# Kernel optimization log

Hardware: AMD Instinct MI355X
Metric: run time of the kernel (lower is better)

## Reference

```python
import jax, jax.numpy as jnp
import numpy as np

SINK = 4          # sink_size: tokens never evicted
MAX_CACHE = 8192  # sink_size + window_size
H = 32            # n_heads
HD = 128          # head_dim
D = H * HD        # d_model


def setup_inputs() -> dict:
    key = jax.random.key(0)
    ks = jax.random.split(key, 7)
    x = jax.random.normal(ks[0], (1, 1, D), dtype=jnp.float32)
    cached_k = jax.random.normal(ks[1], (1, H, MAX_CACHE, HD), dtype=jnp.float32)
    cached_v = jax.random.normal(ks[2], (1, H, MAX_CACHE, HD), dtype=jnp.float32)
    scale = 0.02
    Wq = jax.random.normal(ks[3], (D, D), dtype=jnp.float32) * scale
    Wk = jax.random.normal(ks[4], (D, D), dtype=jnp.float32) * scale
    Wv = jax.random.normal(ks[5], (D, D), dtype=jnp.float32) * scale
    Wo = jax.random.normal(ks[6], (D, D), dtype=jnp.float32) * scale
    return {"x": x, "cached_k": cached_k, "cached_v": cached_v,
            "Wq": Wq, "Wk": Wk, "Wv": Wv, "Wo": Wo}


def reference(x, cached_k, cached_v, Wq, Wk, Wv, Wo):
    """One StreamingLLM decode step with a full sink+window KV cache.

    x:        (1, 1, D)   single new token
    cached_k: (1, H, T, HD) with T == MAX_CACHE (cache at capacity)
    Returns (out, new_cached_k, new_cached_v) where out is (1, 1, D) and the
    new caches reflect sink-preserving eviction: [sink | recent[1:] | new].
    """
    B, S, _ = x.shape  # S == 1
    # projections for the new token -> (B, H, S, HD)
    q = (x @ Wq).reshape(B, S, H, HD).transpose(0, 2, 1, 3)
    k_new = (x @ Wk).reshape(B, S, H, HD).transpose(0, 2, 1, 3)
    v_new = (x @ Wv).reshape(B, S, H, HD).transpose(0, 2, 1, 3)

    # attend over past cache + new token (causal: single query sees everything)
    keys = jnp.concatenate([cached_k, k_new], axis=2)   # (B, H, T+1, HD)
    vals = jnp.concatenate([cached_v, v_new], axis=2)
    inv_sqrt_d = np.float32(1.0 / np.sqrt(HD))
    scores = jnp.einsum('bhqd,bhkd->bhqk', q, keys) * inv_sqrt_d
    attn = jax.nn.softmax(scores, axis=-1)
    ctx = jnp.einsum('bhqk,bhkd->bhqd', attn, vals)     # (B, H, 1, HD)
    out = ctx.transpose(0, 2, 1, 3).reshape(B, S, H * HD) @ Wo

    # KVCache.update full-cache branch: keep sink, drop oldest recent, append new
    new_cached_k = jnp.concatenate(
        [cached_k[:, :, :SINK], cached_k[:, :, SINK + 1:], k_new], axis=2)
    new_cached_v = jnp.concatenate(
        [cached_v[:, :, :SINK], cached_v[:, :, SINK + 1:], v_new], axis=2)
    return out, new_cached_k, new_cached_v
```

## Files before the change

kernel.cpp:

```cpp
#include <hip/hip_runtime.h>

#define D     4096
#define NH    32
#define HD    128
#define TT    8192
#define SINKN 4
#define NC    64
#define CS    (TT / NC)
#define ICH   32
#define IROWS (D / ICH)

__global__ void qkv_partial(const float* __restrict__ x,
                            const float* __restrict__ Wq,
                            const float* __restrict__ Wk,
                            const float* __restrict__ Wv,
                            float* __restrict__ partA) {
    int bid = blockIdx.x;
    int mat = bid / (4 * ICH);
    int rem = bid % (4 * ICH);
    int jb  = rem / ICH;
    int ic  = rem % ICH;
    const float* Wm = (mat == 0) ? Wq : (mat == 1) ? Wk : Wv;
    int tid = threadIdx.x;
    int j0  = jb * 1024 + tid * 4;
    int i0  = ic * IROWS;
    __shared__ float xs[IROWS];
    if (tid < IROWS) xs[tid] = x[i0 + tid];
    __syncthreads();
    float4 acc = {0.f, 0.f, 0.f, 0.f};
    const float* Wp = Wm + (size_t)i0 * D + j0;
    for (int i = 0; i < IROWS; ++i) {
        float4 w = *(const float4*)Wp;
        float xv = xs[i];
        acc.x += xv * w.x; acc.y += xv * w.y;
        acc.z += xv * w.z; acc.w += xv * w.w;
        Wp += D;
    }
    *(float4*)(partA + ((size_t)(mat * ICH + ic)) * D + j0) = acc;
}

__global__ void qkv_reduce(const float* __restrict__ partA,
                           float* __restrict__ qkv,
                           float* __restrict__ newK,
                           float* __restrict__ newV) {
    int idx = blockIdx.x * 256 + threadIdx.x;
    int mat = idx / D;
    int j   = idx % D;
    const float* p = partA + (size_t)mat * ICH * D + j;
    float s = 0.f;
    #pragma unroll
    for (int ic = 0; ic < ICH; ++ic) s += p[(size_t)ic * D];
    qkv[idx] = s;
    if (mat == 1) {
        int h = j / HD, d = j % HD;
        newK[((size_t)h * TT + (TT - 1)) * HD + d] = s;
    } else if (mat == 2) {
        int h = j / HD, d = j % HD;
        newV[((size_t)h * TT + (TT - 1)) * HD + d] = s;
    }
}

__global__ void attn_chunk(const float* __restrict__ q,
                           const float* __restrict__ K,
                           const float* __restrict__ V,
                           float* __restrict__ newK,
                           float* __restrict__ newV,
                           float* __restrict__ partB) {
    int bid = blockIdx.x;
    int h = bid / NC;
    int c = bid % NC;
    int t0 = c * CS;
    int tid  = threadIdx.x;
    int wave = tid >> 6;
    int lane = tid & 63;
    __shared__ float qs[HD];
    __shared__ float sc[CS];
    __shared__ float ml[2];
    __shared__ float ctx4[4][HD];
    if (tid < HD) qs[tid] = q[h * HD + tid];
    __syncthreads();
    float q0 = qs[2 * lane], q1 = qs[2 * lane + 1];
    const float inv_sqrt_d = 0.08838834764831845f;

    const float* Kh = K    + (size_t)h * TT * HD;
    float*      nKh = newK + (size_t)h * TT * HD;
    for (int kk = 0; kk < CS / 4; ++kk) {
        int t = t0 + kk * 4 + wave;
        const float2 kv = *(const float2*)(Kh + (size_t)t * HD + 2 * lane);
        float p = q0 * kv.x + q1 * kv.y;
        #pragma unroll
        for (int off = 32; off; off >>= 1) p += __shfl_xor(p, off, 64);
        if (lane == 0) sc[t - t0] = p * inv_sqrt_d;
        if (t != SINKN) {
            int dst = (t < SINKN) ? t : t - 1;
            *(float2*)(nKh + (size_t)dst * HD + 2 * lane) = kv;
        }
    }
    __syncthreads();
    if (wave == 0) {
        float s0 = sc[lane], s1 = sc[lane + 64];
        float m = fmaxf(s0, s1);
        #pragma unroll
        for (int off = 32; off; off >>= 1) m = fmaxf(m, __shfl_xor(m, off, 64));
        float w0 = __expf(s0 - m), w1 = __expf(s1 - m);
        sc[lane] = w0; sc[lane + 64] = w1;
        float l = w0 + w1;
        #pragma unroll
        for (int off = 32; off; off >>= 1) l += __shfl_xor(l, off, 64);
        if (lane == 0) { ml[0] = m; ml[1] = l; }
    }
    __syncthreads();
    const float* Vh = V    + (size_t)h * TT * HD;
    float*      nVh = newV + (size_t)h * TT * HD;
    float a0 = 0.f, a1 = 0.f;
    for (int kk = 0; kk < CS / 4; ++kk) {
        int t = t0 + kk * 4 + wave;
        const float2 vv = *(const float2*)(Vh + (size_t)t * HD + 2 * lane);
        float w = sc[t - t0];
        a0 += w * vv.x; a1 += w * vv.y;
        if (t != SINKN) {
            int dst = (t < SINKN) ? t : t - 1;
            *(float2*)(nVh + (size_t)dst * HD + 2 * lane) = vv;
        }
    }
    ctx4[wave][2 * lane]     = a0;
    ctx4[wave][2 * lane + 1] = a1;
    __syncthreads();
    float* pb = partB + ((size_t)h * NC + c) * (HD + 2);
    if (tid < HD)
        pb[2 + tid] = ctx4[0][tid] + ctx4[1][tid] + ctx4[2][tid] + ctx4[3][tid];
    if (tid == 0) { pb[0] = ml[0]; pb[1] = ml[1]; }
}

__global__ void attn_combine(const float* __restrict__ q,
                             const float* __restrict__ knew,
                             const float* __restrict__ vnew,
                             const float* __restrict__ partB,
                             float* __restrict__ ctx) {
    int h = blockIdx.x;
    int tid = threadIdx.x;
    __shared__ float red[HD];
    __shared__ float marr[NC], larr[NC];
    red[tid] = q[h * HD + tid] * knew[h * HD + tid];
    __syncthreads();
    for (int s = 64; s > 0; s >>= 1) {
        if (tid < s) red[tid] += red[tid + s];
        __syncthreads();
    }
    float s_new = red[0] * 0.08838834764831845f;
    const float* pb = partB + (size_t)h * NC * (HD + 2);
    if (tid < NC) {
        marr[tid] = pb[(size_t)tid * (HD + 2)];
        larr[tid] = pb[(size_t)tid * (HD + 2) + 1];
    }
    __syncthreads();
    float M = s_new;
    for (int c = 0; c < NC; ++c) M = fmaxf(M, marr[c]);
    float wn = __expf(s_new - M);
    float L = wn;
    for (int c = 0; c < NC; ++c) L += larr[c] * __expf(marr[c] - M);
    float acc = wn * vnew[h * HD + tid];
    for (int c = 0; c < NC; ++c)
        acc += __expf(marr[c] - M) * pb[(size_t)c * (HD + 2) + 2 + tid];
    ctx[h * HD + tid] = acc / L;
}

__global__ void out_partial(const float* __restrict__ ctx,
                            const float* __restrict__ Wo,
                            float* __restrict__ partA) {
    int bid = blockIdx.x;
    int jb = bid / ICH, ic = bid % ICH;
    int tid = threadIdx.x;
    int j0 = jb * 1024 + tid * 4;
    int i0 = ic * IROWS;
    __shared__ float xs[IROWS];
    if (tid < IROWS) xs[tid] = ctx[i0 + tid];
    __syncthreads();
    float4 acc = {0.f, 0.f, 0.f, 0.f};
    const float* Wp = Wo + (size_t)i0 * D + j0;
    for (int i = 0; i < IROWS; ++i) {
        float4 w = *(const float4*)Wp;
        float xv = xs[i];
        acc.x += xv * w.x; acc.y += xv * w.y;
        acc.z += xv * w.z; acc.w += xv * w.w;
        Wp += D;
    }
    *(float4*)(partA + (size_t)ic * D + j0) = acc;
}

__global__ void out_reduce(const float* __restrict__ partA,
                           float* __restrict__ out) {
    int j = blockIdx.x * 256 + threadIdx.x;
    float s = 0.f;
    #pragma unroll
    for (int ic = 0; ic < ICH; ++ic) s += partA[(size_t)ic * D + j];
    out[j] = s;
}

extern "C" void kernel_launch(void* const* d_in, const int* in_sizes, int n_in,
                              void* d_out, int out_size, void* d_ws, size_t ws_size,
                              hipStream_t stream) {
    const float* x  = (const float*)d_in[0];
    const float* cK = (const float*)d_in[1];
    const float* cV = (const float*)d_in[2];
    const float* Wq = (const float*)d_in[3];
    const float* Wk = (const float*)d_in[4];
    const float* Wv = (const float*)d_in[5];
    const float* Wo = (const float*)d_in[6];

    float* out  = (float*)d_out;
    float* newK = out + D;
    float* newV = newK + (size_t)NH * TT * HD;

    float* ws    = (float*)d_ws;
    float* q     = ws;
    float* kn    = ws + D;
    float* vn    = ws + 2 * D;
    float* ctx   = ws + 3 * D;
    float* partA = ws + 4 * D;
    float* partB = partA + 3 * ICH * D;

    qkv_partial <<<3 * 4 * ICH, 256, 0, stream>>>(x, Wq, Wk, Wv, partA);
    qkv_reduce  <<<3 * D / 256, 256, 0, stream>>>(partA, q, newK, newV);
    attn_chunk  <<<NH * NC,     256, 0, stream>>>(q, cK, cV, newK, newV, partB);
    attn_combine<<<NH,          HD,  0, stream>>>(q, kn, vn, partB, ctx);
    out_partial <<<4 * ICH,     256, 0, stream>>>(ctx, Wo, partA);
    out_reduce  <<<D / 256,     256, 0, stream>>>(partA, out);
}
```

Baseline: 192.8 us.

## Fuse QKV reduction into attention kernels and widen attention loads to float4

Removes the separate qkv_reduce launch: attn_chunk now sums the QKV partials for its head's query itself, and attn_combine sums the q/k/v partials and writes the new K/V rows into the cache. The attention loop switches from float2 to float4 loads with two rows per wave, and the combine step precomputes exp factors in shared memory. The projection GEMV kernels use 128-thread blocks with more blocks and unrolling, and the output projection splits into 64 row-chunks. The cost is that every attention block redundantly re-reduces the query partials (2048 blocks, 32 loads each).

Measured after the change: 189.9 us. About the same (-1.5%).

```diff
diff --git a/kernel.cpp b/kernel.cpp
--- a/kernel.cpp
+++ b/kernel.cpp
@@ -8,7 +8,7 @@
 #define NC    64
 #define CS    (TT / NC)
 #define ICH   32
-#define IROWS (D / ICH)
+#define ICHO  64
 
 __global__ void qkv_partial(const float* __restrict__ x,
                             const float* __restrict__ Wq,
@@ -16,51 +16,31 @@
                             const float* __restrict__ Wv,
                             float* __restrict__ partA) {
     int bid = blockIdx.x;
-    int mat = bid / (4 * ICH);
-    int rem = bid % (4 * ICH);
-    int jb  = rem / ICH;
-    int ic  = rem % ICH;
+    int mat = bid / 256;
+    int rem = bid % 256;
+    int jb  = rem >> 5;
+    int ic  = rem & 31;
     const float* Wm = (mat == 0) ? Wq : (mat == 1) ? Wk : Wv;
     int tid = threadIdx.x;
-    int j0  = jb * 1024 + tid * 4;
-    int i0  = ic * IROWS;
-    __shared__ float xs[IROWS];
-    if (tid < IROWS) xs[tid] = x[i0 + tid];
+    int j0  = jb * 512 + tid * 4;
+    int i0  = ic * 128;
+    __shared__ float xs[128];
+    xs[tid] = x[i0 + tid];
     __syncthreads();
     float4 acc = {0.f, 0.f, 0.f, 0.f};
     const float* Wp = Wm + (size_t)i0 * D + j0;
-    for (int i = 0; i < IROWS; ++i) {
+    #pragma unroll 8
+    for (int i = 0; i < 128; ++i) {
         float4 w = *(const float4*)Wp;
         float xv = xs[i];
         acc.x += xv * w.x; acc.y += xv * w.y;
         acc.z += xv * w.z; acc.w += xv * w.w;
         Wp += D;
     }
-    *(float4*)(partA + ((size_t)(mat * ICH + ic)) * D + j0) = acc;
-}
-
-__global__ void qkv_reduce(const float* __restrict__ partA,
-                           float* __restrict__ qkv,
-                           float* __restrict__ newK,
-                           float* __restrict__ newV) {
-    int idx = blockIdx.x * 256 + threadIdx.x;
-    int mat = idx / D;
-    int j   = idx % D;
-    const float* p = partA + (size_t)mat * ICH * D + j;
-    float s = 0.f;
-    #pragma unroll
-    for (int ic = 0; ic < ICH; ++ic) s += p[(size_t)ic * D];
-    qkv[idx] = s;
-    if (mat == 1) {
-        int h = j / HD, d = j % HD;
-        newK[((size_t)h * TT + (TT - 1)) * HD + d] = s;
-    } else if (mat == 2) {
-        int h = j / HD, d = j % HD;
-        newV[((size_t)h * TT + (TT - 1)) * HD + d] = s;
-    }
-}
-
-__global__ void attn_chunk(const float* __restrict__ q,
+    *(float4*)(partA + (size_t)(mat * ICH + ic) * D + j0) = acc;
+}
+
+__global__ void attn_chunk(const float* __restrict__ partA,
                            const float* __restrict__ K,
                            const float* __restrict__ V,
                            float* __restrict__ newK,
@@ -73,27 +53,45 @@
     int tid  = threadIdx.x;
     int wave = tid >> 6;
     int lane = tid & 63;
+    int l31  = lane & 31;
+    int half = lane >> 5;
+
     __shared__ float qs[HD];
     __shared__ float sc[CS];
     __shared__ float ml[2];
-    __shared__ float ctx4[4][HD];
-    if (tid < HD) qs[tid] = q[h * HD + tid];
-    __syncthreads();
-    float q0 = qs[2 * lane], q1 = qs[2 * lane + 1];
-    const float inv_sqrt_d = 0.08838834764831845f;
+    __shared__ float ctx8[8][HD];
+
+    {
+        int d  = tid & 127;
+        int hh = tid >> 7;
+        const float* p = partA + (size_t)(hh * 16) * D + (size_t)h * HD + d;
+        float s = 0.f;
+        #pragma unroll
+        for (int ic = 0; ic < 16; ++ic) s += p[(size_t)ic * D];
+        ctx8[hh][d] = s;
+    }
+    __syncthreads();
+    if (tid < HD) qs[tid] = ctx8[0][tid] + ctx8[1][tid];
+    __syncthreads();
+
+    float4 qv = *(const float4*)(qs + 4 * l31);
+    const float scale = 0.08838834764831845f;
 
     const float* Kh = K    + (size_t)h * TT * HD;
     float*      nKh = newK + (size_t)h * TT * HD;
-    for (int kk = 0; kk < CS / 4; ++kk) {
-        int t = t0 + kk * 4 + wave;
-        const float2 kv = *(const float2*)(Kh + (size_t)t * HD + 2 * lane);
-        float p = q0 * kv.x + q1 * kv.y;
-        #pragma unroll
-        for (int off = 32; off; off >>= 1) p += __shfl_xor(p, off, 64);
-        if (lane == 0) sc[t - t0] = p * inv_sqrt_d;
-        if (t != SINKN) {
-            int dst = (t < SINKN) ? t : t - 1;
-            *(float2*)(nKh + (size_t)dst * HD + 2 * lane) = kv;
+    for (int kk = 0; kk < 16; ++kk) {
+        int r = t0 + kk * 8 + wave * 2 + half;
+        float4 kv = *(const float4*)(Kh + (size_t)r * HD + 4 * l31);
+        float p = qv.x * kv.x + qv.y * kv.y + qv.z * kv.z + qv.w * kv.w;
+        p += __shfl_xor(p, 16, 64);
+        p += __shfl_xor(p, 8, 64);
+        p += __shfl_xor(p, 4, 64);
+        p += __shfl_xor(p, 2, 64);
+        p += __shfl_xor(p, 1, 64);
+        if (l31 == 0) sc[r - t0] = p * scale;
+        if (r != SINKN) {
+            int dst = (r < SINKN) ? r : r - 1;
+            *(float4*)(nKh + (size_t)dst * HD + 4 * l31) = kv;
         }
     }
     __syncthreads();
@@ -112,36 +110,54 @@
     __syncthreads();
     const float* Vh = V    + (size_t)h * TT * HD;
     float*      nVh = newV + (size_t)h * TT * HD;
-    float a0 = 0.f, a1 = 0.f;
-    for (int kk = 0; kk < CS / 4; ++kk) {
-        int t = t0 + kk * 4 + wave;
-        const float2 vv = *(const float2*)(Vh + (size_t)t * HD + 2 * lane);
-        float w = sc[t - t0];
-        a0 += w * vv.x; a1 += w * vv.y;
-        if (t != SINKN) {
-            int dst = (t < SINKN) ? t : t - 1;
-            *(float2*)(nVh + (size_t)dst * HD + 2 * lane) = vv;
+    float a0 = 0.f, a1 = 0.f, a2 = 0.f, a3 = 0.f;
+    for (int kk = 0; kk < 16; ++kk) {
+        int r = t0 + kk * 8 + wave * 2 + half;
+        float4 vv = *(const float4*)(Vh + (size_t)r * HD + 4 * l31);
+        float w = sc[r - t0];
+        a0 += w * vv.x; a1 += w * vv.y; a2 += w * vv.z; a3 += w * vv.w;
+        if (r != SINKN) {
+            int dst = (r < SINKN) ? r : r - 1;
+            *(float4*)(nVh + (size_t)dst * HD + 4 * l31) = vv;
         }
     }
-    ctx4[wave][2 * lane]     = a0;
-    ctx4[wave][2 * lane + 1] = a1;
+    int g = wave * 2 + half;
+    ctx8[g][4 * l31 + 0] = a0;
+    ctx8[g][4 * l31 + 1] = a1;
+    ctx8[g][4 * l31 + 2] = a2;
+    ctx8[g][4 * l31 + 3] = a3;
     __syncthreads();
     float* pb = partB + ((size_t)h * NC + c) * (HD + 2);
-    if (tid < HD)
-        pb[2 + tid] = ctx4[0][tid] + ctx4[1][tid] + ctx4[2][tid] + ctx4[3][tid];
+    if (tid < HD) {
+        float s = 0.f;
+        #pragma unroll
+        for (int gg = 0; gg < 8; ++gg) s += ctx8[gg][tid];
+        pb[2 + tid] = s;
+    }
     if (tid == 0) { pb[0] = ml[0]; pb[1] = ml[1]; }
 }
 
-__global__ void attn_combine(const float* __restrict__ q,
-                             const float* __restrict__ knew,
-                             const float* __restrict__ vnew,
+__global__ void attn_combine(const float* __restrict__ partA,
                              const float* __restrict__ partB,
+                             float* __restrict__ newK,
+                             float* __restrict__ newV,
                              float* __restrict__ ctx) {
     int h = blockIdx.x;
     int tid = threadIdx.x;
+    float qd = 0.f, kd = 0.f, vd = 0.f;
+    const float* pq = partA + (size_t)h * HD + tid;
+    #pragma unroll
+    for (int ic = 0; ic < ICH; ++ic) {
+        qd += pq[(size_t)ic * D];
+        kd += pq[(size_t)(ICH + ic) * D];
+        vd += pq[(size_t)(2 * ICH + ic) * D];
+    }
+    newK[((size_t)h * TT + (TT - 1)) * HD + tid] = kd;
+    newV[((size_t)h * TT + (TT - 1)) * HD + tid] = vd;
+
     __shared__ float red[HD];
-    __shared__ float marr[NC], larr[NC];
-    red[tid] = q[h * HD + tid] * knew[h * HD + tid];
+    __shared__ float marr[NC], larr[NC], earr[NC];
+    red[tid] = qd * kd;
     __syncthreads();
     for (int s = 64; s > 0; s >>= 1) {
         if (tid < s) red[tid] += red[tid + s];
@@ -156,44 +172,48 @@
     __syncthreads();
     float M = s_new;
     for (int c = 0; c < NC; ++c) M = fmaxf(M, marr[c]);
+    if (tid < NC) earr[tid] = __expf(marr[tid] - M);
+    __syncthreads();
     float wn = __expf(s_new - M);
     float L = wn;
-    for (int c = 0; c < NC; ++c) L += larr[c] * __expf(marr[c] - M);
-    float acc = wn * vnew[h * HD + tid];
+    for (int c = 0; c < NC; ++c) L += larr[c] * earr[c];
+    float acc = wn * vd;
     for (int c = 0; c < NC; ++c)
-        acc += __expf(marr[c] - M) * pb[(size_t)c * (HD + 2) + 2 + tid];
+        acc += earr[c] * pb[(size_t)c * (HD + 2) + 2 + tid];
     ctx[h * HD + tid] = acc / L;
 }
 
 __global__ void out_partial(const float* __restrict__ ctx,
                             const float* __restrict__ Wo,
-                            float* __restrict__ partA) {
+                            float* __restrict__ partC) {
     int bid = blockIdx.x;
-    int jb = bid / ICH, ic = bid % ICH;
+    int jb = bid >> 6;
+    int ic = bid & 63;
     int tid = threadIdx.x;
-    int j0 = jb * 1024 + tid * 4;
-    int i0 = ic * IROWS;
-    __shared__ float xs[IROWS];
-    if (tid < IROWS) xs[tid] = ctx[i0 + tid];
+    int j0 = jb * 512 + tid * 4;
+    int i0 = ic * 64;
+    __shared__ float xs[64];
+    if (tid < 64) xs[tid] = ctx[i0 + tid];
     __syncthreads();
     float4 acc = {0.f, 0.f, 0.f, 0.f};
     const float* Wp = Wo + (size_t)i0 * D + j0;
-    for (int i = 0; i < IROWS; ++i) {
+    #pragma unroll 8
+    for (int i = 0; i < 64; ++i) {
         float4 w = *(const float4*)Wp;
         float xv = xs[i];
         acc.x += xv * w.x; acc.y += xv * w.y;
         acc.z += xv * w.z; acc.w += xv * w.w;
         Wp += D;
     }
-    *(float4*)(partA + (size_t)ic * D + j0) = acc;
-}
-
-__global__ void out_reduce(const float* __restrict__ partA,
+    *(float4*)(partC + (size_t)ic * D + j0) = acc;
+}
+
+__global__ void out_reduce(const float* __restrict__ partC,
                            float* __restrict__ out) {
     int j = blockIdx.x * 256 + threadIdx.x;
     float s = 0.f;
     #pragma unroll
-    for (int ic = 0; ic < ICH; ++ic) s += partA[(size_t)ic * D + j];
+    for (int ic = 0; ic < ICHO; ++ic) s += partC[(size_t)ic * D + j];
     out[j] = s;
 }
 
@@ -213,17 +233,13 @@
     float* newV = newK + (size_t)NH * TT * HD;
 
     float* ws    = (float*)d_ws;
-    float* q     = ws;
-    float* kn    = ws + D;
-    float* vn    = ws + 2 * D;
-    float* ctx   = ws + 3 * D;
-    float* partA = ws + 4 * D;
+    float* partA = ws;
     float* partB = partA + 3 * ICH * D;
-
-    qkv_partial <<<3 * 4 * ICH, 256, 0, stream>>>(x, Wq, Wk, Wv, partA);
-    qkv_reduce  <<<3 * D / 256, 256, 0, stream>>>(partA, q, newK, newV);
-    attn_chunk  <<<NH * NC,     256, 0, stream>>>(q, cK, cV, newK, newV, partB);
-    attn_combine<<<NH,          HD,  0, stream>>>(q, kn, vn, partB, ctx);
-    out_partial <<<4 * ICH,     256, 0, stream>>>(ctx, Wo, partA);
-    out_reduce  <<<D / 256,     256, 0, stream>>>(partA, out);
-}
+    float* ctx   = partB + NH * NC * (HD + 2);
+
+    qkv_partial <<<768,  128, 0, stream>>>(x, Wq, Wk, Wv, partA);
+    attn_chunk  <<<NH * NC, 256, 0, stream>>>(partA, cK, cV, newK, newV, partB);
+    attn_combine<<<NH,   HD,  0, stream>>>(partA, partB, newK, newV, ctx);
+    out_partial <<<512,  128, 0, stream>>>(ctx, Wo, partA);
+    out_reduce  <<<D / 256, 256, 0, stream>>>(partA, out);
+}
```
